# Kernel tuning notes

Hardware: AMD Instinct MI355X
Metric: run time of the kernel (lower is better)

The kernel has to match this reference:

```python
import jax, jax.numpy as jnp
import numpy as np

NEG = -1e9
LRELU_ALPHA = 0.2  # tf.nn.leaky_relu default


def setup_inputs() -> dict:
    key = jax.random.key(0)
    k = jax.random.split(key, 6)
    B, N, F_in, F_out = 1, 8192, 256, 64
    x = jax.random.normal(k[0], (B, N, F_in), dtype=jnp.float32)
    # sparse adjacency as additive bias: ~32 neighbors/node on average
    u = jax.random.uniform(k[1], (B, N, N), dtype=jnp.float32)
    adj = jnp.where(u < 32.0 / N, 0.0, NEG).astype(jnp.float32)
    W = jax.random.normal(k[2], (F_in, F_out), dtype=jnp.float32) * (1.0 / np.sqrt(F_in))
    a1 = jax.random.normal(k[3], (F_out, 1), dtype=jnp.float32) * (1.0 / np.sqrt(F_out))
    a2 = jax.random.normal(k[4], (F_out, 1), dtype=jnp.float32) * (1.0 / np.sqrt(F_out))
    b1 = jnp.zeros((1,), dtype=jnp.float32)
    b2 = jnp.zeros((1,), dtype=jnp.float32)
    bias = jnp.zeros((F_out,), dtype=jnp.float32)
    return {"x": x, "adj": adj, "W": W, "a1": a1, "b1": b1, "a2": a2, "b2": b2, "bias": bias}


def reference(x, adj, W, a1, b1, a2, b2, bias):
    # conv1 (kernel_size=1, no bias) == per-node linear projection
    fts = jnp.einsum('bnf,fo->bno', x, W)            # [B, N, F_out]
    f1 = jnp.einsum('bno,oi->bni', fts, a1) + b1     # [B, N, 1]
    f2 = jnp.einsum('bno,oi->bni', fts, a2) + b2     # [B, N, 1]
    logits = f1 + jnp.swapaxes(f2, 1, 2)             # [B, N, N] additive scores
    scores = jax.nn.leaky_relu(logits, LRELU_ALPHA) + adj
    coefs = jax.nn.softmax(scores, axis=-1)          # [B, N, N]
    vals = jnp.einsum('bnm,bmo->bno', coefs, fts) + bias
    return jax.nn.elu(vals)
```

## Files before the change

### kernel.cpp

```cpp
#include <hip/hip_runtime.h>
#include <cstdint>

#define N_NODES 8192
#define F_IN    256
#define F_OUT   64
#define ALPHA   0.2f
#define SCAN_BLOCKS 2048
#define CAPG    128

__global__ __launch_bounds__(256) void k_proj(const float* __restrict__ x,
                                              const float* __restrict__ W,
                                              const float* __restrict__ a1,
                                              const float* __restrict__ b1,
                                              const float* __restrict__ a2,
                                              const float* __restrict__ b2,
                                              float* __restrict__ fts,
                                              float* __restrict__ f1,
                                              float* __restrict__ f2) {
    __shared__ __align__(16) float ws[64][F_OUT];
    const int t = threadIdx.x, lane = t & 63, w = t >> 6;
    const int rowA = blockIdx.x * 8 + w * 2;
    const int rowB = rowA + 1;

    const float4* xqA = (const float4*)(x + (size_t)rowA * F_IN);
    const float4* xqB = (const float4*)(x + (size_t)rowB * F_IN);
    float accA = 0.f, accB = 0.f;

    for (int kc = 0; kc < 4; ++kc) {
        if (kc) __syncthreads();
        {
            const float4* Wt = (const float4*)(W + (size_t)kc * 64 * F_OUT);
            float4* S = (float4*)&ws[0][0];
            S[t]       = Wt[t];
            S[t + 256] = Wt[t + 256];
            S[t + 512] = Wt[t + 512];
            S[t + 768] = Wt[t + 768];
        }
        __syncthreads();
        #pragma unroll
        for (int q = 0; q < 16; ++q) {
            const float4 xa = xqA[kc * 16 + q];
            const float4 xb = xqB[kc * 16 + q];
            const float w0 = ws[q*4+0][lane];
            const float w1 = ws[q*4+1][lane];
            const float w2 = ws[q*4+2][lane];
            const float w3 = ws[q*4+3][lane];
            accA += xa.x*w0 + xa.y*w1 + xa.z*w2 + xa.w*w3;
            accB += xb.x*w0 + xb.y*w1 + xb.z*w2 + xb.w*w3;
        }
    }
    fts[(size_t)rowA * F_OUT + lane] = accA;
    fts[(size_t)rowB * F_OUT + lane] = accB;

    const float u1 = a1[lane], u2 = a2[lane];
    float sA1 = accA * u1, sA2 = accA * u2;
    float sB1 = accB * u1, sB2 = accB * u2;
    #pragma unroll
    for (int off = 32; off >= 1; off >>= 1) {
        sA1 += __shfl_xor(sA1, off, 64);
        sA2 += __shfl_xor(sA2, off, 64);
        sB1 += __shfl_xor(sB1, off, 64);
        sB2 += __shfl_xor(sB2, off, 64);
    }
    if (lane == 0) {
        const float bb1 = b1[0], bb2 = b2[0];
        f1[rowA] = sA1 + bb1;  f2[rowA] = sA2 + bb2;
        f1[rowB] = sB1 + bb1;  f2[rowB] = sB2 + bb2;
    }
}

__global__ __launch_bounds__(256) void k_bits(const float* __restrict__ adj,
                                              unsigned long long* __restrict__ bm) {
    const int S = SCAN_BLOCKS * 256;
    const float4* A = (const float4*)adj;
    const int lane = threadIdx.x & 63;
    int q = blockIdx.x * 256 + threadIdx.x;

    #pragma unroll 1
    for (int it = 0; it < 8; ++it) {
        const float4 v0 = A[q];
        const float4 v1 = A[q + S];
        const float4 v2 = A[q + 2 * S];
        const float4 v3 = A[q + 3 * S];

        const unsigned long long b0 = __ballot(fmaxf(fmaxf(fmaxf(v0.x, v0.y), v0.z), v0.w) > -0.5f);
        const unsigned long long b1 = __ballot(fmaxf(fmaxf(fmaxf(v1.x, v1.y), v1.z), v1.w) > -0.5f);
        const unsigned long long b2 = __ballot(fmaxf(fmaxf(fmaxf(v2.x, v2.y), v2.z), v2.w) > -0.5f);
        const unsigned long long b3 = __ballot(fmaxf(fmaxf(fmaxf(v3.x, v3.y), v3.z), v3.w) > -0.5f);

        if (lane == 0) {
            bm[q >> 6]           = b0;
            bm[(q + S) >> 6]     = b1;
            bm[(q + 2 * S) >> 6] = b2;
            bm[(q + 3 * S) >> 6] = b3;
        }
        q += 4 * S;
    }
}

__global__ __launch_bounds__(256) void k_gather(const unsigned long long* __restrict__ bm,
                                                const float* __restrict__ adj,
                                                const float* __restrict__ fts,
                                                const float* __restrict__ f1,
                                                const float* __restrict__ f2,
                                                const float* __restrict__ bias,
                                                float* __restrict__ out) {
    __shared__ int lj[4][CAPG];
    __shared__ int lcnt[4];

    const int lane = threadIdx.x & 63, w = threadIdx.x >> 6;
    const int row  = blockIdx.x * 4 + w;
    if (threadIdx.x < 4) lcnt[threadIdx.x] = 0;
    __syncthreads();

    unsigned long long wv = 0;
    if (lane < 32) wv = bm[row * 32 + lane];
    const float4* A4 = (const float4*)adj;
    while (wv) {
        const int b = __ffsll((long long)wv) - 1;
        wv &= wv - 1;
        const int ql = (lane << 6) + b;
        const float4 av = A4[(size_t)row * 2048 + ql];
        if (av.x > -0.5f) { int p = atomicAdd(&lcnt[w], 1); if (p < CAPG) lj[w][p] = 4*ql+0; }
        if (av.y > -0.5f) { int p = atomicAdd(&lcnt[w], 1); if (p < CAPG) lj[w][p] = 4*ql+1; }
        if (av.z > -0.5f) { int p = atomicAdd(&lcnt[w], 1); if (p < CAPG) lj[w][p] = 4*ql+2; }
        if (av.w > -0.5f) { int p = atomicAdd(&lcnt[w], 1); if (p < CAPG) lj[w][p] = 4*ql+3; }
    }
    __syncthreads();

    int n = lcnt[w];
    n = (n < CAPG) ? n : CAPG;
    const float f1r = f1[row];

    float l0 = -3.0e38f, l1 = -3.0e38f;
    int   j0 = 0, j1 = 0;
    if (lane < n)      { j0 = lj[w][lane];      const float g = f1r + f2[j0]; l0 = fmaxf(g, ALPHA * g); }
    if (lane + 64 < n) { j1 = lj[w][lane + 64]; const float g = f1r + f2[j1]; l1 = fmaxf(g, ALPHA * g); }

    float m = fmaxf(l0, l1);
    #pragma unroll
    for (int off = 32; off >= 1; off >>= 1)
        m = fmaxf(m, __shfl_xor(m, off, 64));

    const float p0 = __expf(l0 - m);
    const float p1 = __expf(l1 - m);

    float den = p0 + p1;
    #pragma unroll
    for (int off = 32; off >= 1; off >>= 1)
        den += __shfl_xor(den, off, 64);

    float acc = 0.f;
    {
        const int nb = (n < 64) ? n : 64;
        for (int k = 0; k < nb; ++k)
            acc += __shfl(p0, k, 64) * fts[(size_t)__shfl(j0, k, 64) * F_OUT + lane];
    }
    if (n > 64) {
        const int nb = n - 64;
        for (int k = 0; k < nb; ++k)
            acc += __shfl(p1, k, 64) * fts[(size_t)__shfl(j1, k, 64) * F_OUT + lane];
    }

    const float v = acc / den + bias[lane];
    out[(size_t)row * F_OUT + lane] = (v > 0.f) ? v : expm1f(v);
}

extern "C" void kernel_launch(void* const* d_in, const int* in_sizes, int n_in,
                              void* d_out, int out_size, void* d_ws, size_t ws_size,
                              hipStream_t stream) {
    const float* x    = (const float*)d_in[0];
    const float* adj  = (const float*)d_in[1];
    const float* W    = (const float*)d_in[2];
    const float* a1   = (const float*)d_in[3];
    const float* b1   = (const float*)d_in[4];
    const float* a2   = (const float*)d_in[5];
    const float* b2   = (const float*)d_in[6];
    const float* bias = (const float*)d_in[7];
    float* out = (float*)d_out;

    float* fts = (float*)d_ws;
    float* f1  = fts + (size_t)N_NODES * F_OUT;
    float* f2  = f1 + N_NODES;
    unsigned long long* bm = (unsigned long long*)(f2 + N_NODES);

    k_bits  <<<SCAN_BLOCKS, 256, 0, stream>>>(adj, bm);
    k_proj  <<<N_NODES / 8, 256, 0, stream>>>(x, W, a1, b1, a2, b2, fts, f1, f2);
    k_gather<<<N_NODES / 4, 256, 0, stream>>>(bm, adj, fts, f1, f2, bias, out);
}
```

Measured before the change: 419.2 us.

## Fuse adjacency bitmap scan into gather kernel with per-wave ballot compaction

Removes the separate bitmap kernel and has each wave stream its own adjacency row directly with nontemporal vector loads. Neighbour indices are compacted with ballots and a wave-uniform counter instead of shared-memory atomics. This drops one kernel launch, the bitmap write and read, and the second read of adjacency rows, at the cost of serial per-bit loops inside the scan and less memory-level parallelism per wave than the grid-wide scan had. The neighbour order becomes column-ordered per component rather than atomic-order, which can change float summation order slightly.

```diff
diff --git a/kernel.cpp b/kernel.cpp
--- a/kernel.cpp
+++ b/kernel.cpp
@@ -5,8 +5,9 @@
 #define F_IN    256
 #define F_OUT   64
 #define ALPHA   0.2f
-#define SCAN_BLOCKS 2048
 #define CAPG    128
+
+typedef float f32x4 __attribute__((ext_vector_type(4)));
 
 __global__ __launch_bounds__(256) void k_proj(const float* __restrict__ x,
                                               const float* __restrict__ W,
@@ -69,67 +70,53 @@
     }
 }
 
-__global__ __launch_bounds__(256) void k_bits(const float* __restrict__ adj,
-                                              unsigned long long* __restrict__ bm) {
-    const int S = SCAN_BLOCKS * 256;
-    const float4* A = (const float4*)adj;
-    const int lane = threadIdx.x & 63;
-    int q = blockIdx.x * 256 + threadIdx.x;
-
-    #pragma unroll 1
-    for (int it = 0; it < 8; ++it) {
-        const float4 v0 = A[q];
-        const float4 v1 = A[q + S];
-        const float4 v2 = A[q + 2 * S];
-        const float4 v3 = A[q + 3 * S];
-
-        const unsigned long long b0 = __ballot(fmaxf(fmaxf(fmaxf(v0.x, v0.y), v0.z), v0.w) > -0.5f);
-        const unsigned long long b1 = __ballot(fmaxf(fmaxf(fmaxf(v1.x, v1.y), v1.z), v1.w) > -0.5f);
-        const unsigned long long b2 = __ballot(fmaxf(fmaxf(fmaxf(v2.x, v2.y), v2.z), v2.w) > -0.5f);
-        const unsigned long long b3 = __ballot(fmaxf(fmaxf(fmaxf(v3.x, v3.y), v3.z), v3.w) > -0.5f);
-
-        if (lane == 0) {
-            bm[q >> 6]           = b0;
-            bm[(q + S) >> 6]     = b1;
-            bm[(q + 2 * S) >> 6] = b2;
-            bm[(q + 3 * S) >> 6] = b3;
-        }
-        q += 4 * S;
-    }
-}
-
-__global__ __launch_bounds__(256) void k_gather(const unsigned long long* __restrict__ bm,
-                                                const float* __restrict__ adj,
-                                                const float* __restrict__ fts,
-                                                const float* __restrict__ f1,
-                                                const float* __restrict__ f2,
-                                                const float* __restrict__ bias,
-                                                float* __restrict__ out) {
+__global__ __launch_bounds__(256) void k_mega(const float* __restrict__ adj,
+                                              const float* __restrict__ fts,
+                                              const float* __restrict__ f1,
+                                              const float* __restrict__ f2,
+                                              const float* __restrict__ bias,
+                                              float* __restrict__ out) {
     __shared__ int lj[4][CAPG];
-    __shared__ int lcnt[4];
 
     const int lane = threadIdx.x & 63, w = threadIdx.x >> 6;
     const int row  = blockIdx.x * 4 + w;
-    if (threadIdx.x < 4) lcnt[threadIdx.x] = 0;
-    __syncthreads();
+    const f32x4* Ar = (const f32x4*)(adj + (size_t)row * N_NODES);
 
-    unsigned long long wv = 0;
-    if (lane < 32) wv = bm[row * 32 + lane];
-    const float4* A4 = (const float4*)adj;
-    while (wv) {
-        const int b = __ffsll((long long)wv) - 1;
-        wv &= wv - 1;
-        const int ql = (lane << 6) + b;
-        const float4 av = A4[(size_t)row * 2048 + ql];
-        if (av.x > -0.5f) { int p = atomicAdd(&lcnt[w], 1); if (p < CAPG) lj[w][p] = 4*ql+0; }
-        if (av.y > -0.5f) { int p = atomicAdd(&lcnt[w], 1); if (p < CAPG) lj[w][p] = 4*ql+1; }
-        if (av.z > -0.5f) { int p = atomicAdd(&lcnt[w], 1); if (p < CAPG) lj[w][p] = 4*ql+2; }
-        if (av.w > -0.5f) { int p = atomicAdd(&lcnt[w], 1); if (p < CAPG) lj[w][p] = 4*ql+3; }
+    int cnt = 0;
+    #pragma unroll 1
+    for (int cb = 0; cb < 2048; cb += 256) {
+        const f32x4 v0 = __builtin_nontemporal_load(&Ar[cb + lane]);
+        const f32x4 v1 = __builtin_nontemporal_load(&Ar[cb + 64 + lane]);
+        const f32x4 v2 = __builtin_nontemporal_load(&Ar[cb + 128 + lane]);
+        const f32x4 v3 = __builtin_nontemporal_load(&Ar[cb + 192 + lane]);
+
+        #define SCAN4(v, qb)                                                          \
+        {                                                                             \
+            unsigned long long mx = __ballot((v)[0] > -0.5f);                         \
+            unsigned long long my = __ballot((v)[1] > -0.5f);                         \
+            unsigned long long mz = __ballot((v)[2] > -0.5f);                         \
+            unsigned long long mw = __ballot((v)[3] > -0.5f);                         \
+            while (mx) { const int l = __ffsll((long long)mx) - 1; mx &= mx - 1;      \
+                if (lane == 0 && cnt < CAPG) lj[w][cnt] = (((qb) + l) << 2) | 0;      \
+                ++cnt; }                                                              \
+            while (my) { const int l = __ffsll((long long)my) - 1; my &= my - 1;      \
+                if (lane == 0 && cnt < CAPG) lj[w][cnt] = (((qb) + l) << 2) | 1;      \
+                ++cnt; }                                                              \
+            while (mz) { const int l = __ffsll((long long)mz) - 1; mz &= mz - 1;      \
+                if (lane == 0 && cnt < CAPG) lj[w][cnt] = (((qb) + l) << 2) | 2;      \
+                ++cnt; }                                                              \
+            while (mw) { const int l = __ffsll((long long)mw) - 1; mw &= mw - 1;      \
+                if (lane == 0 && cnt < CAPG) lj[w][cnt] = (((qb) + l) << 2) | 3;      \
+                ++cnt; }                                                              \
+        }
+        SCAN4(v0, cb)
+        SCAN4(v1, cb + 64)
+        SCAN4(v2, cb + 128)
+        SCAN4(v3, cb + 192)
+        #undef SCAN4
     }
-    __syncthreads();
 
-    int n = lcnt[w];
-    n = (n < CAPG) ? n : CAPG;
+    const int n = (cnt < CAPG) ? cnt : CAPG;
     const float f1r = f1[row];
 
     float l0 = -3.0e38f, l1 = -3.0e38f;
@@ -182,9 +169,7 @@
     float* fts = (float*)d_ws;
     float* f1  = fts + (size_t)N_NODES * F_OUT;
     float* f2  = f1 + N_NODES;
-    unsigned long long* bm = (unsigned long long*)(f2 + N_NODES);
 
-    k_bits  <<<SCAN_BLOCKS, 256, 0, stream>>>(adj, bm);
-    k_proj  <<<N_NODES / 8, 256, 0, stream>>>(x, W, a1, b1, a2, b2, fts, f1, f2);
-    k_gather<<<N_NODES / 4, 256, 0, stream>>>(bm, adj, fts, f1, f2, bias, out);
+    k_proj<<<N_NODES / 8, 256, 0, stream>>>(x, W, a1, b1, a2, b2, fts, f1, f2);
+    k_mega<<<N_NODES / 4, 256, 0, stream>>>(adj, fts, f1, f2, bias, out);
 }
```

Result: faster. 384.2 us (-8.3%).
